# Optimization experiments

Measured on AMD Instinct MI355X. Metric: run time of the kernel, lower is better.

Reference implementation:

```python
import jax, jax.numpy as jnp
import numpy as np

B, S, D, E, K = 4, 2048, 1024, 8, 2
H = 4 * D  # FFN hidden per expert


def setup_inputs() -> dict:
    key = jax.random.key(0)
    ks = jax.random.split(key, 5)
    s = 0.02  # init scale
    return {
        "x": jax.random.normal(ks[0], (B, S, D), dtype=jnp.float32),
        "Wg": jax.random.normal(ks[1], (D, E), dtype=jnp.float32) * s,
        "bg": jnp.zeros((E,), dtype=jnp.float32),
        "W1": jax.random.normal(ks[2], (E, D, H), dtype=jnp.float32) * s,
        "b1": jnp.zeros((E, H), dtype=jnp.float32),
        "W2": jax.random.normal(ks[3], (E, H, D), dtype=jnp.float32) * s,
        "b2": jnp.zeros((E, D), dtype=jnp.float32),
    }


def reference(x, Wg, bg, W1, b1, W2, b2):
    # Router: softmax over expert logits, then top-k (torch.topk semantics)
    probs = jax.nn.softmax(x @ Wg + bg, axis=-1)      # [B,S,E]
    w, idx = jax.lax.top_k(probs, K)                   # [B,S,K] each
    # Dense all-experts MLP (matches original: every expert runs on every token)
    h = jax.nn.gelu(jnp.einsum('bsd,edh->bseh', x, W1) + b1, approximate=False)  # [B,S,E,H]
    y = jnp.einsum('bseh,ehd->bsed', h, W2) + b2       # [B,S,E,D]
    # One-hot mask + weighted sum == gather selected experts, scale by w, sum over k
    yk = jnp.take_along_axis(y, idx[..., None], axis=2)  # [B,S,K,D]
    return jnp.sum(yk * w[..., None], axis=2)            # [B,S,D]
```

## Files before the change

kernel.cpp:

```cpp
#include <hip/hip_runtime.h>
#include <hip/hip_bf16.h>
#include <math.h>


#define TOK     8192
#define DMODEL  1024
#define NEXP    8
#define HFF     4096
#define NASSIGN 16384
#define SLOTPAD 16512
#define BM      128
#define BN      128
#define BK      64
#define MAXRT   135

typedef __attribute__((ext_vector_type(8))) short s16x8;
typedef __attribute__((ext_vector_type(4))) float f32x4;

__device__ __forceinline__ void gll16(const void* g, void* l) {
  __builtin_amdgcn_global_load_lds((const __attribute__((address_space(1))) void*)g,
                                   (__attribute__((address_space(3))) void*)l, 16, 0, 0);
}

__global__ void transpose_cvt(const float* __restrict__ W1, const float* __restrict__ W2,
                              __hip_bfloat16* __restrict__ W1t, __hip_bfloat16* __restrict__ W2t) {
  __shared__ float t[64][65];
  const int z = blockIdx.y;
  const float* src; __hip_bfloat16* dst; int R, C, bx, by;
  if (z < 8) {
    R = DMODEL; C = HFF;
    src = W1 + (size_t)z * R * C; dst = W1t + (size_t)z * R * C;
    bx = blockIdx.x & 63; by = blockIdx.x >> 6;
  } else {
    R = HFF; C = DMODEL;
    src = W2 + (size_t)(z - 8) * R * C; dst = W2t + (size_t)(z - 8) * R * C;
    bx = blockIdx.x & 15; by = blockIdx.x >> 4;
  }
  const int r0 = by * 64, c0 = bx * 64;
  const int tc = threadIdx.x & 63, tr = threadIdx.x >> 6;
#pragma unroll
  for (int i = 0; i < 16; ++i) {
    int r = i * 4 + tr;
    t[r][tc] = src[(size_t)(r0 + r) * C + c0 + tc];
  }
  __syncthreads();
  const int jl = (threadIdx.x & 15) * 4;
  const int cw = threadIdx.x >> 4;
#pragma unroll
  for (int p = 0; p < 4; ++p) {
    const int cc = p * 16 + cw;
    union { ushort4 u; __hip_bfloat16 h[4]; } o;
#pragma unroll
    for (int u = 0; u < 4; ++u) o.h[u] = __float2bfloat16(t[jl + u][cc]);
    *(ushort4*)(dst + (size_t)(c0 + cc) * R + r0 + jl) = o.u;
  }
}

__global__ void router_kernel(const float* __restrict__ x, const float* __restrict__ Wg,
                              const float* __restrict__ bg, int* __restrict__ idx,
                              float* __restrict__ wtok, int* ctrl) {
  __shared__ int scnt[NEXP];
  if (threadIdx.x < NEXP) scnt[threadIdx.x] = 0;
  __syncthreads();
  const int wave = threadIdx.x >> 6, lane = threadIdx.x & 63;
  const int t = blockIdx.x * 4 + wave;
  float acc[NEXP];
#pragma unroll
  for (int e = 0; e < NEXP; ++e) acc[e] = 0.f;
  const float* xr = x + (size_t)t * DMODEL + lane * 16;
#pragma unroll
  for (int j = 0; j < 4; ++j) {
    float4 xv = *(const float4*)(xr + j * 4);
    const float* wr = Wg + (size_t)(lane * 16 + j * 4) * NEXP;
#pragma unroll
    for (int u = 0; u < 4; ++u) {
      float xs = (&xv.x)[u];
      float4 w0 = *(const float4*)(wr + u * NEXP);
      float4 w1 = *(const float4*)(wr + u * NEXP + 4);
      acc[0] += xs * w0.x; acc[1] += xs * w0.y; acc[2] += xs * w0.z; acc[3] += xs * w0.w;
      acc[4] += xs * w1.x; acc[5] += xs * w1.y; acc[6] += xs * w1.z; acc[7] += xs * w1.w;
    }
  }
#pragma unroll
  for (int off = 32; off >= 1; off >>= 1) {
#pragma unroll
    for (int e = 0; e < NEXP; ++e) acc[e] += __shfl_xor(acc[e], off, 64);
  }
  if (lane == 0) {
    float l[NEXP], m = -1e30f;
#pragma unroll
    for (int e = 0; e < NEXP; ++e) { l[e] = acc[e] + bg[e]; m = fmaxf(m, l[e]); }
    float p[NEXP], s = 0.f;
#pragma unroll
    for (int e = 0; e < NEXP; ++e) { p[e] = expf(l[e] - m); s += p[e]; }
    float inv = 1.f / s;
#pragma unroll
    for (int e = 0; e < NEXP; ++e) p[e] *= inv;
    int i0 = 0; float v0 = p[0];
#pragma unroll
    for (int e = 1; e < NEXP; ++e) if (p[e] > v0) { v0 = p[e]; i0 = e; }
    int i1 = -1; float v1 = -1e30f;
#pragma unroll
    for (int e = 0; e < NEXP; ++e) if (e != i0 && p[e] > v1) { v1 = p[e]; i1 = e; }
    idx[2 * t] = i0; idx[2 * t + 1] = i1;
    wtok[2 * t] = v0; wtok[2 * t + 1] = v1;
    atomicAdd(&scnt[i0], 1); atomicAdd(&scnt[i1], 1);
  }
  __syncthreads();
  if (threadIdx.x < NEXP) atomicAdd(&ctrl[threadIdx.x], scnt[threadIdx.x]);
  if (threadIdx.x == 0) {
    __threadfence();
    const int done = atomicAdd(&ctrl[63], 1);
    if (done == (int)gridDim.x - 1) {
      int c[NEXP];
#pragma unroll
      for (int e = 0; e < NEXP; ++e) c[e] = atomicAdd(&ctrl[e], 0);
      int eo = 0, tr = 0;
      ctrl[16] = 0; ctrl[26] = 0;
#pragma unroll
      for (int e = 0; e < NEXP; ++e) {
        ctrl[8 + e] = eo;
        eo += c[e]; tr += (c[e] + BM - 1) / BM;
        ctrl[17 + e] = eo;
        ctrl[27 + e] = tr;
      }
    }
  }
}

__global__ void scatter_kernel(const int* __restrict__ idx, const float* __restrict__ wtok,
                               int* ctrl, int* __restrict__ perm, int* __restrict__ ts,
                               float* __restrict__ wslot) {
  __shared__ int lcnt[NEXP];
  __shared__ int lbase[NEXP];
  const int t = blockIdx.x * 256 + threadIdx.x;
  if (threadIdx.x < NEXP) lcnt[threadIdx.x] = 0;
  __syncthreads();
  const int e0 = idx[2 * t], e1 = idx[2 * t + 1];
  const int l0 = atomicAdd(&lcnt[e0], 1);
  const int l1 = atomicAdd(&lcnt[e1], 1);
  __syncthreads();
  if (threadIdx.x < NEXP)
    lbase[threadIdx.x] = atomicAdd(&ctrl[8 + threadIdx.x], lcnt[threadIdx.x]);
  __syncthreads();
  const int s0 = lbase[e0] + l0, s1 = lbase[e1] + l1;
  perm[s0] = t; perm[s1] = t;
  ts[2 * t] = s0; ts[2 * t + 1] = s1;
  wslot[s0] = wtok[2 * t]; wslot[s1] = wtok[2 * t + 1];
}

__global__ void gather_cvt_x(const float* __restrict__ x, const int* __restrict__ perm,
                             __hip_bfloat16* __restrict__ xg) {
  const int slot = blockIdx.x;
  const int t = perm[slot];
  const float4 v = *(const float4*)(x + (size_t)t * DMODEL + threadIdx.x * 4);
  union { ushort4 u; __hip_bfloat16 h[4]; } o;
  o.h[0] = __float2bfloat16(v.x); o.h[1] = __float2bfloat16(v.y);
  o.h[2] = __float2bfloat16(v.z); o.h[3] = __float2bfloat16(v.w);
  *(ushort4*)(xg + (size_t)slot * DMODEL + threadIdx.x * 4) = o.u;
}


__global__ __launch_bounds__(256, 2) void gemm1_kernel(
    const __hip_bfloat16* __restrict__ xg, const __hip_bfloat16* __restrict__ w1t,
    const float* __restrict__ b1, __hip_bfloat16* __restrict__ hbuf,
    const int* __restrict__ ctrl) {
  const int* expOff = ctrl + 16;
  const int* tro = ctrl + 26;
  const int w = blockIdx.x;
  const int rt = w >> 5, nt = w & 31;
  if (rt >= tro[NEXP]) return;
  int e = 0;
#pragma unroll
  for (int q = 1; q < NEXP; ++q) if (tro[q] <= rt) e = q;
  const int rowBase = expOff[e] + (rt - tro[e]) * BM;
  const int rowEnd = expOff[e + 1];

  __shared__ __hip_bfloat16 lA[2 * BM * BK];
  __shared__ __hip_bfloat16 lB[2 * BN * BK];

  const int tid = threadIdx.x;
  const int lane = tid & 63, wave = tid >> 6;
  const int quad = lane >> 4, lm = lane & 15;
  const int waveM = (wave >> 1) * 64, waveN = (wave & 1) * 64;

  f32x4 acc[4][4];
#pragma unroll
  for (int a = 0; a < 4; ++a)
#pragma unroll
    for (int b = 0; b < 4; ++b) acc[a][b] = (f32x4){0.f, 0.f, 0.f, 0.f};

  const __hip_bfloat16* bbase = w1t + (size_t)e * HFF * DMODEL + (size_t)nt * BN * DMODEL;
  const __hip_bfloat16* gA[4]; const __hip_bfloat16* gB[4];
#pragma unroll
  for (int i = 0; i < 4; ++i) {
    const int s = tid + 256 * i;
    const int r = s >> 3, sl = s & 7, kc = sl ^ (r & 7);
    gA[i] = xg + (size_t)(rowBase + r) * DMODEL + kc * 8;
    gB[i] = bbase + (size_t)r * DMODEL + kc * 8;
  }

  int aOff[4], bOff[4];
#pragma unroll
  for (int tm = 0; tm < 4; ++tm) {
    int r = waveM + tm * 16 + lm;
    aOff[tm] = r * 64 + (quad ^ (r & 7)) * 8;
  }
#pragma unroll
  for (int tn = 0; tn < 4; ++tn) {
    int r = waveN + tn * 16 + lm;
    bOff[tn] = r * 64 + (quad ^ (r & 7)) * 8;
  }

#pragma unroll
  for (int i = 0; i < 4; ++i) {
    gll16(gA[i], lA + tid * 8 + i * 2048);
    gll16(gB[i], lB + tid * 8 + i * 2048);
    gA[i] += BK; gB[i] += BK;
  }
  __syncthreads();

  const int NTI = DMODEL / BK;
  for (int kt = 0; kt < NTI; ++kt) {
    if (kt + 1 < NTI) {
      const int nb = (kt + 1) & 1;
#pragma unroll
      for (int i = 0; i < 4; ++i) {
        gll16(gA[i], lA + nb * 8192 + tid * 8 + i * 2048);
        gll16(gB[i], lB + nb * 8192 + tid * 8 + i * 2048);
        gA[i] += BK; gB[i] += BK;
      }
    }
    const __hip_bfloat16* ba = lA + (kt & 1) * 8192;
    const __hip_bfloat16* bb = lB + (kt & 1) * 8192;
    s16x8 af[2][4], bfr[2][4];
#pragma unroll
    for (int h = 0; h < 2; ++h) {
#pragma unroll
      for (int tm = 0; tm < 4; ++tm) af[h][tm] = *(const s16x8*)(ba + (aOff[tm] ^ (h * 32)));
#pragma unroll
      for (int tn = 0; tn < 4; ++tn) bfr[h][tn] = *(const s16x8*)(bb + (bOff[tn] ^ (h * 32)));
    }
    __builtin_amdgcn_s_setprio(1);
#pragma unroll
    for (int h = 0; h < 2; ++h)
#pragma unroll
      for (int tm = 0; tm < 4; ++tm)
#pragma unroll
        for (int tn = 0; tn < 4; ++tn)
          acc[tm][tn] = __builtin_amdgcn_mfma_f32_16x16x32_bf16(af[h][tm], bfr[h][tn],
                                                                acc[tm][tn], 0, 0, 0);
    __builtin_amdgcn_s_setprio(0);
    if (kt + 1 < NTI) __syncthreads();
  }

  const int colBase = nt * BN + waveN;
  float bv[4];
#pragma unroll
  for (int tn = 0; tn < 4; ++tn) bv[tn] = b1[e * HFF + colBase + tn * 16 + lm];
#pragma unroll
  for (int tm = 0; tm < 4; ++tm) {
    const int rb = rowBase + waveM + tm * 16 + quad * 4;
#pragma unroll
    for (int reg = 0; reg < 4; ++reg) {
      const int row = rb + reg;
      if (row < rowEnd) {
#pragma unroll
        for (int tn = 0; tn < 4; ++tn) {
          float v = acc[tm][tn][reg] + bv[tn];
          v = 0.5f * v * (1.f + erff(v * 0.70710678118654752f));
          hbuf[(size_t)row * HFF + colBase + tn * 16 + lm] = __float2bfloat16(v);
        }
      }
    }
  }
}

__global__ __launch_bounds__(256, 2) void gemm2_kernel(
    const __hip_bfloat16* __restrict__ hbuf, const __hip_bfloat16* __restrict__ w2t,
    const float* __restrict__ b2, const float* __restrict__ wslot,
    float* __restrict__ y, const int* __restrict__ ctrl) {
  const int* expOff = ctrl + 16;
  const int* tro = ctrl + 26;
  const int w = blockIdx.x;
  const int rt = w >> 3, nt = w & 7;
  if (rt >= tro[NEXP]) return;
  int e = 0;
#pragma unroll
  for (int q = 1; q < NEXP; ++q) if (tro[q] <= rt) e = q;
  const int rowBase = expOff[e] + (rt - tro[e]) * BM;
  const int rowEnd = expOff[e + 1];

  __shared__ __hip_bfloat16 lA[2 * BM * BK];
  __shared__ __hip_bfloat16 lB[2 * BN * BK];

  const int tid = threadIdx.x;
  const int lane = tid & 63, wave = tid >> 6;
  const int quad = lane >> 4, lm = lane & 15;
  const int waveM = (wave >> 1) * 64, waveN = (wave & 1) * 64;

  f32x4 acc[4][4];
#pragma unroll
  for (int a = 0; a < 4; ++a)
#pragma unroll
    for (int b = 0; b < 4; ++b) acc[a][b] = (f32x4){0.f, 0.f, 0.f, 0.f};

  const __hip_bfloat16* bbase = w2t + (size_t)e * DMODEL * HFF + (size_t)nt * BN * HFF;
  const __hip_bfloat16* gA[4]; const __hip_bfloat16* gB[4];
#pragma unroll
  for (int i = 0; i < 4; ++i) {
    const int s = tid + 256 * i;
    const int r = s >> 3, sl = s & 7, kc = sl ^ (r & 7);
    gA[i] = hbuf + (size_t)(rowBase + r) * HFF + kc * 8;
    gB[i] = bbase + (size_t)r * HFF + kc * 8;
  }

  int aOff[4], bOff[4];
#pragma unroll
  for (int tm = 0; tm < 4; ++tm) {
    int r = waveM + tm * 16 + lm;
    aOff[tm] = r * 64 + (quad ^ (r & 7)) * 8;
  }
#pragma unroll
  for (int tn = 0; tn < 4; ++tn) {
    int r = waveN + tn * 16 + lm;
    bOff[tn] = r * 64 + (quad ^ (r & 7)) * 8;
  }

#pragma unroll
  for (int i = 0; i < 4; ++i) {
    gll16(gA[i], lA + tid * 8 + i * 2048);
    gll16(gB[i], lB + tid * 8 + i * 2048);
    gA[i] += BK; gB[i] += BK;
  }
  __syncthreads();

  const int NTI = HFF / BK;
  for (int kt = 0; kt < NTI; ++kt) {
    if (kt + 1 < NTI) {
      const int nb = (kt + 1) & 1;
#pragma unroll
      for (int i = 0; i < 4; ++i) {
        gll16(gA[i], lA + nb * 8192 + tid * 8 + i * 2048);
        gll16(gB[i], lB + nb * 8192 + tid * 8 + i * 2048);
        gA[i] += BK; gB[i] += BK;
      }
    }
    const __hip_bfloat16* ba = lA + (kt & 1) * 8192;
    const __hip_bfloat16* bb = lB + (kt & 1) * 8192;
    s16x8 af[2][4], bfr[2][4];
#pragma unroll
    for (int h = 0; h < 2; ++h) {
#pragma unroll
      for (int tm = 0; tm < 4; ++tm) af[h][tm] = *(const s16x8*)(ba + (aOff[tm] ^ (h * 32)));
#pragma unroll
      for (int tn = 0; tn < 4; ++tn) bfr[h][tn] = *(const s16x8*)(bb + (bOff[tn] ^ (h * 32)));
    }
    __builtin_amdgcn_s_setprio(1);
#pragma unroll
    for (int h = 0; h < 2; ++h)
#pragma unroll
      for (int tm = 0; tm < 4; ++tm)
#pragma unroll
        for (int tn = 0; tn < 4; ++tn)
          acc[tm][tn] = __builtin_amdgcn_mfma_f32_16x16x32_bf16(af[h][tm], bfr[h][tn],
                                                                acc[tm][tn], 0, 0, 0);
    __builtin_amdgcn_s_setprio(0);
    if (kt + 1 < NTI) __syncthreads();
  }

  const int colBase = nt * BN + waveN;
  float bv[4];
#pragma unroll
  for (int tn = 0; tn < 4; ++tn) bv[tn] = b2[e * DMODEL + colBase + tn * 16 + lm];
#pragma unroll
  for (int tm = 0; tm < 4; ++tm) {
    const int rb = rowBase + waveM + tm * 16 + quad * 4;
#pragma unroll
    for (int reg = 0; reg < 4; ++reg) {
      const int row = rb + reg;
      if (row < rowEnd) {
        const float wr = wslot[row];
        float* yr = y + (size_t)row * DMODEL + colBase;
#pragma unroll
        for (int tn = 0; tn < 4; ++tn)
          yr[tn * 16 + lm] = (acc[tm][tn][reg] + bv[tn]) * wr;
      }
    }
  }
}

__global__ void combine_kernel(const float* __restrict__ y, const int* __restrict__ ts,
                               float* __restrict__ out) {
  const int t = blockIdx.x;
  const int s0 = ts[2 * t], s1 = ts[2 * t + 1];
  const int c = threadIdx.x * 4;
  const float4 a = *(const float4*)(y + (size_t)s0 * DMODEL + c);
  const float4 b = *(const float4*)(y + (size_t)s1 * DMODEL + c);
  float4 r; r.x = a.x + b.x; r.y = a.y + b.y; r.z = a.z + b.z; r.w = a.w + b.w;
  *(float4*)(out + (size_t)t * DMODEL + c) = r;
}

extern "C" void kernel_launch(void* const* d_in, const int* in_sizes, int n_in,
                              void* d_out, int out_size, void* d_ws, size_t ws_size,
                              hipStream_t stream) {
  const float* x  = (const float*)d_in[0];
  const float* Wg = (const float*)d_in[1];
  const float* bg = (const float*)d_in[2];
  const float* W1 = (const float*)d_in[3];
  const float* b1 = (const float*)d_in[4];
  const float* W2 = (const float*)d_in[5];
  const float* b2 = (const float*)d_in[6];
  float* out = (float*)d_out;

  char* ws = (char*)d_ws;
  size_t off = 0;
  auto take = [&](size_t bytes) -> char* {
    char* p = ws + off;
    off = (off + bytes + 255) & ~(size_t)255;
    return p;
  };
  int*   ctrl  = (int*)take(64 * sizeof(int));
  int*   idx   = (int*)take((size_t)TOK * 2 * 4);
  float* wtok  = (float*)take((size_t)TOK * 2 * 4);
  int*   perm  = (int*)take((size_t)SLOTPAD * 4);
  int*   ts    = (int*)take((size_t)TOK * 2 * 4);
  float* wslot = (float*)take((size_t)SLOTPAD * 4);
  __hip_bfloat16* W1t = (__hip_bfloat16*)take((size_t)NEXP * HFF * DMODEL * 2);
  __hip_bfloat16* W2t = (__hip_bfloat16*)take((size_t)NEXP * DMODEL * HFF * 2);
  __hip_bfloat16* xgb = (__hip_bfloat16*)take((size_t)SLOTPAD * DMODEL * 2);
  __hip_bfloat16* hb  = (__hip_bfloat16*)take((size_t)SLOTPAD * HFF * 2);
  float* y = (float*)W1t;
  (void)ws_size; (void)in_sizes; (void)n_in; (void)out_size;

  hipMemsetAsync(ctrl, 0, 64 * sizeof(int), stream);
  transpose_cvt<<<dim3(1024, 16), 256, 0, stream>>>(W1, W2, W1t, W2t);
  router_kernel<<<TOK / 4, 256, 0, stream>>>(x, Wg, bg, idx, wtok, ctrl);
  scatter_kernel<<<TOK / 256, 256, 0, stream>>>(idx, wtok, ctrl, perm, ts, wslot);
  gather_cvt_x<<<NASSIGN, 256, 0, stream>>>(x, perm, xgb);
  gemm1_kernel<<<MAXRT * (HFF / BN), 256, 0, stream>>>(xgb, W1t, b1, hb, ctrl);
  gemm2_kernel<<<MAXRT * (DMODEL / BN), 256, 0, stream>>>(hb, W2t, b2, wslot, y, ctrl);
  combine_kernel<<<TOK, 256, 0, stream>>>(y, ts, out);
}
```

Baseline: 982.0 us.

## Single-buffer LDS in expert GEMMs and raise occupancy to four blocks per CU

Both grouped GEMM kernels move from double-buffered LDS tiles with prefetch to a single LDS buffer. Each k-step now loads, synchronizes and computes in sequence, and fragment loads are split per half-K to lower register pressure. Launch bounds rise from 2 to 4 blocks per CU, so latency is meant to be hidden by more resident waves instead of software pipelining. The risk is that with one buffer, global loads no longer overlap compute inside a block, and two barriers per k-step add sync cost.

```diff
diff --git a/kernel.cpp b/kernel.cpp
--- a/kernel.cpp
+++ b/kernel.cpp
@@ -161,7 +161,7 @@
 }
 
 
-__global__ __launch_bounds__(256, 2) void gemm1_kernel(
+__global__ __launch_bounds__(256, 4) void gemm1_kernel(
     const __hip_bfloat16* __restrict__ xg, const __hip_bfloat16* __restrict__ w1t,
     const float* __restrict__ b1, __hip_bfloat16* __restrict__ hbuf,
     const int* __restrict__ ctrl) {
@@ -176,8 +176,8 @@
   const int rowBase = expOff[e] + (rt - tro[e]) * BM;
   const int rowEnd = expOff[e + 1];
 
-  __shared__ __hip_bfloat16 lA[2 * BM * BK];
-  __shared__ __hip_bfloat16 lB[2 * BN * BK];
+  __shared__ __hip_bfloat16 lA[BM * BK];
+  __shared__ __hip_bfloat16 lB[BN * BK];
 
   const int tid = threadIdx.x;
   const int lane = tid & 63, wave = tid >> 6;
@@ -190,68 +190,45 @@
 #pragma unroll
     for (int b = 0; b < 4; ++b) acc[a][b] = (f32x4){0.f, 0.f, 0.f, 0.f};
 
-  const __hip_bfloat16* bbase = w1t + (size_t)e * HFF * DMODEL + (size_t)nt * BN * DMODEL;
-  const __hip_bfloat16* gA[4]; const __hip_bfloat16* gB[4];
-#pragma unroll
-  for (int i = 0; i < 4; ++i) {
-    const int s = tid + 256 * i;
-    const int r = s >> 3, sl = s & 7, kc = sl ^ (r & 7);
-    gA[i] = xg + (size_t)(rowBase + r) * DMODEL + kc * 8;
-    gB[i] = bbase + (size_t)r * DMODEL + kc * 8;
-  }
-
-  int aOff[4], bOff[4];
-#pragma unroll
-  for (int tm = 0; tm < 4; ++tm) {
-    int r = waveM + tm * 16 + lm;
-    aOff[tm] = r * 64 + (quad ^ (r & 7)) * 8;
-  }
-#pragma unroll
-  for (int tn = 0; tn < 4; ++tn) {
-    int r = waveN + tn * 16 + lm;
-    bOff[tn] = r * 64 + (quad ^ (r & 7)) * 8;
-  }
-
-#pragma unroll
-  for (int i = 0; i < 4; ++i) {
-    gll16(gA[i], lA + tid * 8 + i * 2048);
-    gll16(gB[i], lB + tid * 8 + i * 2048);
-    gA[i] += BK; gB[i] += BK;
-  }
-  __syncthreads();
-
-  const int NTI = DMODEL / BK;
-  for (int kt = 0; kt < NTI; ++kt) {
-    if (kt + 1 < NTI) {
-      const int nb = (kt + 1) & 1;
-#pragma unroll
-      for (int i = 0; i < 4; ++i) {
-        gll16(gA[i], lA + nb * 8192 + tid * 8 + i * 2048);
-        gll16(gB[i], lB + nb * 8192 + tid * 8 + i * 2048);
-        gA[i] += BK; gB[i] += BK;
-      }
-    }
-    const __hip_bfloat16* ba = lA + (kt & 1) * 8192;
-    const __hip_bfloat16* bb = lB + (kt & 1) * 8192;
-    s16x8 af[2][4], bfr[2][4];
+  const __hip_bfloat16* gA0;
+  const __hip_bfloat16* gB0;
+  {
+    const int r = tid >> 3, kc = (tid & 7) ^ (r & 7);
+    gA0 = xg + (size_t)(rowBase + r) * DMODEL + kc * 8;
+    gB0 = w1t + (size_t)e * HFF * DMODEL + (size_t)nt * BN * DMODEL
+              + (size_t)r * DMODEL + kc * 8;
+  }
+
+  const int aO = (waveM + lm) * 64 + ((quad ^ (lm & 7)) << 3);
+  const int bO = (waveN + lm) * 64 + ((quad ^ (lm & 7)) << 3);
+
+  for (int kt = 0; kt < DMODEL / BK; ++kt) {
+#pragma unroll
+    for (int i = 0; i < 4; ++i) {
+      gll16(gA0 + (size_t)(i * 32) * DMODEL, lA + tid * 8 + i * 2048);
+      gll16(gB0 + (size_t)(i * 32) * DMODEL, lB + tid * 8 + i * 2048);
+    }
+    gA0 += BK; gB0 += BK;
+    __syncthreads();
 #pragma unroll
     for (int h = 0; h < 2; ++h) {
-#pragma unroll
-      for (int tm = 0; tm < 4; ++tm) af[h][tm] = *(const s16x8*)(ba + (aOff[tm] ^ (h * 32)));
-#pragma unroll
-      for (int tn = 0; tn < 4; ++tn) bfr[h][tn] = *(const s16x8*)(bb + (bOff[tn] ^ (h * 32)));
-    }
-    __builtin_amdgcn_s_setprio(1);
-#pragma unroll
-    for (int h = 0; h < 2; ++h)
+      const __hip_bfloat16* pa = lA + (aO ^ (h * 32));
+      const __hip_bfloat16* pb = lB + (bO ^ (h * 32));
+      s16x8 af[4], bfr[4];
+#pragma unroll
+      for (int tm = 0; tm < 4; ++tm) af[tm] = *(const s16x8*)(pa + tm * 1024);
+#pragma unroll
+      for (int tn = 0; tn < 4; ++tn) bfr[tn] = *(const s16x8*)(pb + tn * 1024);
+      __builtin_amdgcn_s_setprio(1);
 #pragma unroll
       for (int tm = 0; tm < 4; ++tm)
 #pragma unroll
         for (int tn = 0; tn < 4; ++tn)
-          acc[tm][tn] = __builtin_amdgcn_mfma_f32_16x16x32_bf16(af[h][tm], bfr[h][tn],
+          acc[tm][tn] = __builtin_amdgcn_mfma_f32_16x16x32_bf16(af[tm], bfr[tn],
                                                                 acc[tm][tn], 0, 0, 0);
-    __builtin_amdgcn_s_setprio(0);
-    if (kt + 1 < NTI) __syncthreads();
+      __builtin_amdgcn_s_setprio(0);
+    }
+    __syncthreads();
   }
 
   const int colBase = nt * BN + waveN;
@@ -276,7 +253,7 @@
   }
 }
 
-__global__ __launch_bounds__(256, 2) void gemm2_kernel(
+__global__ __launch_bounds__(256, 4) void gemm2_kernel(
     const __hip_bfloat16* __restrict__ hbuf, const __hip_bfloat16* __restrict__ w2t,
     const float* __restrict__ b2, const float* __restrict__ wslot,
     float* __restrict__ y, const int* __restrict__ ctrl) {
@@ -291,8 +268,8 @@
   const int rowBase = expOff[e] + (rt - tro[e]) * BM;
   const int rowEnd = expOff[e + 1];
 
-  __shared__ __hip_bfloat16 lA[2 * BM * BK];
-  __shared__ __hip_bfloat16 lB[2 * BN * BK];
+  __shared__ __hip_bfloat16 lA[BM * BK];
+  __shared__ __hip_bfloat16 lB[BN * BK];
 
   const int tid = threadIdx.x;
   const int lane = tid & 63, wave = tid >> 6;
@@ -305,68 +282,45 @@
 #pragma unroll
     for (int b = 0; b < 4; ++b) acc[a][b] = (f32x4){0.f, 0.f, 0.f, 0.f};
 
-  const __hip_bfloat16* bbase = w2t + (size_t)e * DMODEL * HFF + (size_t)nt * BN * HFF;
-  const __hip_bfloat16* gA[4]; const __hip_bfloat16* gB[4];
-#pragma unroll
-  for (int i = 0; i < 4; ++i) {
-    const int s = tid + 256 * i;
-    const int r = s >> 3, sl = s & 7, kc = sl ^ (r & 7);
-    gA[i] = hbuf + (size_t)(rowBase + r) * HFF + kc * 8;
-    gB[i] = bbase + (size_t)r * HFF + kc * 8;
-  }
-
-  int aOff[4], bOff[4];
-#pragma unroll
-  for (int tm = 0; tm < 4; ++tm) {
-    int r = waveM + tm * 16 + lm;
-    aOff[tm] = r * 64 + (quad ^ (r & 7)) * 8;
-  }
-#pragma unroll
-  for (int tn = 0; tn < 4; ++tn) {
-    int r = waveN + tn * 16 + lm;
-    bOff[tn] = r * 64 + (quad ^ (r & 7)) * 8;
-  }
-
-#pragma unroll
-  for (int i = 0; i < 4; ++i) {
-    gll16(gA[i], lA + tid * 8 + i * 2048);
-    gll16(gB[i], lB + tid * 8 + i * 2048);
-    gA[i] += BK; gB[i] += BK;
-  }
-  __syncthreads();
-
-  const int NTI = HFF / BK;
-  for (int kt = 0; kt < NTI; ++kt) {
-    if (kt + 1 < NTI) {
-      const int nb = (kt + 1) & 1;
-#pragma unroll
-      for (int i = 0; i < 4; ++i) {
-        gll16(gA[i], lA + nb * 8192 + tid * 8 + i * 2048);
-        gll16(gB[i], lB + nb * 8192 + tid * 8 + i * 2048);
-        gA[i] += BK; gB[i] += BK;
-      }
-    }
-    const __hip_bfloat16* ba = lA + (kt & 1) * 8192;
-    const __hip_bfloat16* bb = lB + (kt & 1) * 8192;
-    s16x8 af[2][4], bfr[2][4];
+  const __hip_bfloat16* gA0;
+  const __hip_bfloat16* gB0;
+  {
+    const int r = tid >> 3, kc = (tid & 7) ^ (r & 7);
+    gA0 = hbuf + (size_t)(rowBase + r) * HFF + kc * 8;
+    gB0 = w2t + (size_t)e * DMODEL * HFF + (size_t)nt * BN * HFF
+              + (size_t)r * HFF + kc * 8;
+  }
+
+  const int aO = (waveM + lm) * 64 + ((quad ^ (lm & 7)) << 3);
+  const int bO = (waveN + lm) * 64 + ((quad ^ (lm & 7)) << 3);
+
+  for (int kt = 0; kt < HFF / BK; ++kt) {
+#pragma unroll
+    for (int i = 0; i < 4; ++i) {
+      gll16(gA0 + (size_t)(i * 32) * HFF, lA + tid * 8 + i * 2048);
+      gll16(gB0 + (size_t)(i * 32) * HFF, lB + tid * 8 + i * 2048);
+    }
+    gA0 += BK; gB0 += BK;
+    __syncthreads();
 #pragma unroll
     for (int h = 0; h < 2; ++h) {
-#pragma unroll
-      for (int tm = 0; tm < 4; ++tm) af[h][tm] = *(const s16x8*)(ba + (aOff[tm] ^ (h * 32)));
-#pragma unroll
-      for (int tn = 0; tn < 4; ++tn) bfr[h][tn] = *(const s16x8*)(bb + (bOff[tn] ^ (h * 32)));
-    }
-    __builtin_amdgcn_s_setprio(1);
-#pragma unroll
-    for (int h = 0; h < 2; ++h)
+      const __hip_bfloat16* pa = lA + (aO ^ (h * 32));
+      const __hip_bfloat16* pb = lB + (bO ^ (h * 32));
+      s16x8 af[4], bfr[4];
+#pragma unroll
+      for (int tm = 0; tm < 4; ++tm) af[tm] = *(const s16x8*)(pa + tm * 1024);
+#pragma unroll
+      for (int tn = 0; tn < 4; ++tn) bfr[tn] = *(const s16x8*)(pb + tn * 1024);
+      __builtin_amdgcn_s_setprio(1);
 #pragma unroll
       for (int tm = 0; tm < 4; ++tm)
 #pragma unroll
         for (int tn = 0; tn < 4; ++tn)
-          acc[tm][tn] = __builtin_amdgcn_mfma_f32_16x16x32_bf16(af[h][tm], bfr[h][tn],
+          acc[tm][tn] = __builtin_amdgcn_mfma_f32_16x16x32_bf16(af[tm], bfr[tn],
                                                                 acc[tm][tn], 0, 0, 0);
-    __builtin_amdgcn_s_setprio(0);
-    if (kt + 1 < NTI) __syncthreads();
+      __builtin_amdgcn_s_setprio(0);
+    }
+    __syncthreads();
   }
 
   const int colBase = nt * BN + waveN;
```

Result: faster. 835.2 us (-15.0%).
